# Kernel optimization log

Hardware: AMD Instinct MI355X
Metric: run time of the kernel (lower is better)

The kernel has to match this reference:

```python
import jax, jax.numpy as jnp
import numpy as np

B, L, D = 16, 2048, 192  # batch, frames_per_data, units
H, K = 4, 12             # num_heads, key_dim (hardcoded in build())
EPS = 1e-3               # keras LayerNormalization default epsilon


def layer_norm(x, g, b):
    m = jnp.mean(x, axis=-1, keepdims=True)
    v = jnp.mean(jnp.square(x - m), axis=-1, keepdims=True)
    return (x - m) * jax.lax.rsqrt(v + EPS) * g + b


def conv1d_valid(x, w, b):
    # x: [B,L,C], w: [3,Cin,Cout] -> [B,L-2,Cout]
    return jax.lax.conv_general_dilated(
        x, w, window_strides=(1,), padding='VALID',
        dimension_numbers=('NWC', 'WIO', 'NWC')) + b


def setup_inputs() -> dict:
    key = jax.random.key(0)
    ks = jax.random.split(key, 16)
    s = 0.05
    return {
        'x': jax.random.normal(ks[0], (B, L, D), jnp.float32),
        'ln1_g': jnp.ones((D,), jnp.float32),
        'ln1_b': jnp.zeros((D,), jnp.float32),
        'wq': jax.random.normal(ks[1], (D, H, K), jnp.float32) * s,
        'bq': jnp.zeros((H, K), jnp.float32),
        'wk': jax.random.normal(ks[2], (D, H, K), jnp.float32) * s,
        'bk': jnp.zeros((H, K), jnp.float32),
        'wv': jax.random.normal(ks[3], (D, H, K), jnp.float32) * s,
        'bv': jnp.zeros((H, K), jnp.float32),
        'wo': jax.random.normal(ks[4], (H, K, D), jnp.float32) * s,
        'bo': jnp.zeros((D,), jnp.float32),
        'ln2_g': jnp.ones((D,), jnp.float32),
        'ln2_b': jnp.zeros((D,), jnp.float32),
        'c1_w': jax.random.normal(ks[5], (3, D, D), jnp.float32) * s,
        'c1_b': jnp.zeros((D,), jnp.float32),
        'c2_w': jax.random.normal(ks[6], (3, D, D), jnp.float32) * s,
        'c2_b': jnp.zeros((D,), jnp.float32),
    }


def reference(x, ln1_g, ln1_b, wq, bq, wk, bk, wv, bv, wo, bo,
              ln2_g, ln2_b, c1_w, c1_b, c2_w, c2_b):
    # --- LN1 + causal MHA + residual (dropout = identity at inference) ---
    xn = layer_norm(x, ln1_g, ln1_b)
    q = jnp.einsum('bld,dhk->blhk', xn, wq) + bq
    k = jnp.einsum('bld,dhk->blhk', xn, wk) + bk
    v = jnp.einsum('bld,dhk->blhk', xn, wv) + bv
    scores = jnp.einsum('blhk,bmhk->bhlm', q, k) / jnp.sqrt(jnp.float32(K))
    causal = jnp.tril(jnp.ones((L, L), jnp.float32))  # tril(True) mask
    scores = scores + (1.0 - causal) * (-1e9)          # keras additive mask
    attn = jax.nn.softmax(scores, axis=-1)
    ctx = jnp.einsum('bhlm,bmhk->blhk', attn, v)
    mha = jnp.einsum('blhk,hkd->bld', ctx, wo) + bo
    x = x + mha
    # --- LN2 + positionwise Conv1D feedforward + residual ---
    xn = layer_norm(x, ln2_g, ln2_b)
    h = jax.nn.relu(conv1d_valid(xn, c1_w, c1_b))      # [B,L-2,D]
    h = jnp.pad(h, ((0, 0), (1, 1), (0, 0)))           # ZeroPadding1D(1,1)
    h = conv1d_valid(h, c2_w, c2_b)                    # [B,L-2,D]
    h = jnp.pad(h, ((0, 0), (1, 1), (0, 0)))
    return x + h
```

## Files before the change

kernel.cpp:

```cpp
#include <hip/hip_runtime.h>
#include <hip/hip_bf16.h>

#define L_ 2048
#define D_ 192
#define HK_ 48
#define EPS_ 1e-3f
#define SCALE_ 0.28867513459481287f
#define LOG2E_ 1.4426950408889634f

typedef __hip_bfloat16 bf16;
typedef _Float16 f16;
typedef __fp16 hf16x2 __attribute__((ext_vector_type(2)));
typedef _Float16 f16x4 __attribute__((ext_vector_type(4)));
typedef __bf16 bf16x8 __attribute__((ext_vector_type(8)));
typedef float  f32x4  __attribute__((ext_vector_type(4)));

__device__ __forceinline__ float b2f(bf16 x) { return __bfloat162float(x); }
__device__ __forceinline__ bf16 f2b(float x) { return __float2bfloat16(x); }

__global__ __launch_bounds__(256) void k_prep_all(
    const float* __restrict__ c1w, const float* __restrict__ c2w,
    const float* __restrict__ wq, const float* __restrict__ wk, const float* __restrict__ wv,
    const float* __restrict__ bq, const float* __restrict__ bk, const float* __restrict__ bv,
    const float* __restrict__ wo,
    bf16* __restrict__ wrep1, bf16* __restrict__ wrep2,
    bf16* __restrict__ wrepq, float* __restrict__ bias144, bf16* __restrict__ wrepo)
{
    const int i = blockIdx.x * 256 + threadIdx.x;
    if (i < 110592) {
        const int k = i / 192, n = i - k * 192;
        wrep1[((size_t)(k >> 5) * 192 + n) * 32 + (k & 31)] = f2b(c1w[i]);
    } else if (i < 221184) {
        const int j = i - 110592;
        const int k = j / 192, n = j - k * 192;
        wrep2[((size_t)(k >> 5) * 192 + n) * 32 + (k & 31)] = f2b(c2w[j]);
    } else if (i < 248832) {
        const int j = i - 221184;
        const int kb = j / 4608, rem = j % 4608;
        const int n = rem / 32, kk = rem % 32;
        const int k = kb * 32 + kk;
        float v;
        if (n < 48)       v = wq[k * HK_ + n] * (SCALE_ * LOG2E_);
        else if (n < 96)  v = wk[k * HK_ + (n - 48)];
        else              v = wv[k * HK_ + (n - 96)];
        wrepq[j] = f2b(v);
    } else if (i < 248976) {
        const int j = i - 248832;
        bias144[j] = (j < 48) ? bq[j] * (SCALE_ * LOG2E_)
                   : (j < 96) ? bk[j - 48] : bv[j - 96];
    } else if (i < 261264) {
        const int j = i - 248976;
        const int kb = j / 6144, rem = j % 6144;
        const int n = rem / 32, kk = rem % 32;
        const int k = kb * 32 + kk;
        wrepo[j] = f2b(k < 48 ? wo[k * D_ + n] : 0.f);
    }
}

__global__ __launch_bounds__(256, 4) void k_ln_qkv(
    const float* __restrict__ x, const float* __restrict__ g1, const float* __restrict__ b1,
    const bf16* __restrict__ wrep, const float* __restrict__ bias144,
    f16* __restrict__ qo, f16* __restrict__ ko, f16* __restrict__ vt)
{
    __shared__ bf16 xn[32 * 200];
    const int tid = threadIdx.x;
    const int wave = tid >> 6, lane = tid & 63;
    const int rowbase = blockIdx.x * 32;
    const int b = rowbase >> 11;
    const int lrow0 = rowbase & 2047;

    const float gg0 = g1[lane], gg1 = g1[lane + 64], gg2 = g1[lane + 128];
    const float bb0 = b1[lane], bb1 = b1[lane + 64], bb2 = b1[lane + 128];
    for (int i = 0; i < 8; ++i) {
        const int r = wave * 8 + i;
        const float* xp = x + (size_t)(rowbase + r) * D_;
        const float x0 = xp[lane];
        const float x1 = xp[lane + 64];
        const float x2 = xp[lane + 128];
        float s = x0 + x1 + x2;
        float q = x0 * x0 + x1 * x1 + x2 * x2;
        #pragma unroll
        for (int m = 1; m < 64; m <<= 1) {
            s += __shfl_xor(s, m, 64);
            q += __shfl_xor(q, m, 64);
        }
        const float mean = s * (1.0f / 192.0f);
        const float var  = q * (1.0f / 192.0f) - mean * mean;
        const float rs   = rsqrtf(var + EPS_);
        xn[r * 200 + lane]       = f2b((x0 - mean) * rs * gg0 + bb0);
        xn[r * 200 + lane + 64]  = f2b((x1 - mean) * rs * gg1 + bb1);
        xn[r * 200 + lane + 128] = f2b((x2 - mean) * rs * gg2 + bb2);
    }

    if (tid < 128) {
        const int h  = tid >> 5;
        const int vc = 12 + ((tid >> 3) & 3);
        const int p0 = lrow0 + (tid & 7) * 4;
        f16x4 vv;
        vv[0] = vv[1] = vv[2] = vv[3] = (vc == 12) ? (f16)1.0f : (f16)0.0f;
        *(f16x4*)(vt + ((size_t)(b * 4 + h) * 16 + vc) * 2048 + p0) = vv;
    }
    __syncthreads();

    const int l15 = lane & 15, q4 = lane >> 4;
    const int rt = wave >> 1, g = wave & 1;
    const int ntlim = 5 - g;
    f32x4 acc[5];
    #pragma unroll
    for (int nt = 0; nt < 5; ++nt) acc[nt] = (f32x4){0.f, 0.f, 0.f, 0.f};

    const bf16* xrow = xn + (rt * 16 + l15) * 200 + q4 * 8;
    #pragma unroll
    for (int kb = 0; kb < 6; ++kb) {
        const bf16x8 a = *(const bf16x8*)(xrow + kb * 32);
        const bf16* wp = wrep + ((size_t)kb * 144 + l15) * 32 + q4 * 8
                       + (size_t)(g * 5) * 16 * 32;
        #pragma unroll
        for (int nt = 0; nt < 5; ++nt) {
            if (nt < ntlim) {
                const bf16x8 bfr = *(const bf16x8*)(wp + (size_t)nt * 16 * 32);
                acc[nt] = __builtin_amdgcn_mfma_f32_16x16x32_bf16(a, bfr, acc[nt], 0, 0, 0);
            }
        }
    }

    const int rw = rowbase + rt * 16 + q4 * 4;
    #pragma unroll
    for (int nt = 0; nt < 5; ++nt) {
        if (nt < ntlim) {
            const int ntg = g * 5 + nt;
            const int col = ntg * 16 + l15;
            const float bd = bias144[col];
            if (ntg < 3) {
                #pragma unroll
                for (int reg = 0; reg < 4; ++reg)
                    qo[(size_t)(rw + reg) * HK_ + col] = (f16)(acc[nt][reg] + bd);
            } else if (ntg < 6) {
                #pragma unroll
                for (int reg = 0; reg < 4; ++reg)
                    ko[(size_t)(rw + reg) * HK_ + (col - 48)] = (f16)(acc[nt][reg] + bd);
            } else {
                const int vcol = col - 96;
                const int h = vcol / 12, c12 = vcol % 12;
                f16x4 vv;
                #pragma unroll
                for (int reg = 0; reg < 4; ++reg) vv[reg] = (f16)(acc[nt][reg] + bd);
                *(f16x4*)(vt + ((size_t)(b * 4 + h) * 16 + c12) * 2048 +
                          lrow0 + rt * 16 + q4 * 4) = vv;
            }
        }
    }
}

__global__ __launch_bounds__(256, 8) void k_attn_part(
    const f16* __restrict__ qh, const f16* __restrict__ kh, const f16* __restrict__ vt,
    bf16* __restrict__ part_o, float* __restrict__ part_l)
{
    const int tid = threadIdx.x;
    const int wv = tid >> 6, lane = tid & 63;
    const int quad = lane >> 4, l15 = lane & 15;
    const int bh = blockIdx.x / 36;
    int r = blockIdx.x % 36;
    int qt = 0;
    while (r >= qt + 1) { r -= qt + 1; ++qt; }
    const int ks = r;
    const int b = bh >> 2, h = bh & 3;
    const size_t base  = (size_t)b * L_ * HK_ + h * 12;
    const size_t vbase = ((size_t)bh * 16 + l15) * 2048;
    const int kbase = ks * 256;
    const int qbase = qt * 256 + wv * 64;
    const bool diag = (ks == qt);
    const int ktmax = diag ? 4 * (wv + 1) : 16;

    f16x4 Qf[4];
    #pragma unroll
    for (int s = 0; s < 4; ++s) {
        f16x4 v;
        if (quad < 3)
            v = *(const f16x4*)(qh + base + (size_t)(qbase + s * 16 + l15) * HK_ + quad * 4);
        else { v[0] = (f16)LOG2E_; v[1] = 0; v[2] = 0; v[3] = 0; }
        Qf[s] = v;
    }

    f32x4 O[4];
    #pragma unroll
    for (int s = 0; s < 4; ++s) O[s] = (f32x4){0.f, 0.f, 0.f, 0.f};

    for (int g = 0; g < ktmax; g += 2) {
        f16x4 Kg[2], Vg[2];
        #pragma unroll
        for (int u = 0; u < 2; ++u) {
            const int kt = g + u;
            f16x4 kf;
            if (quad < 3)
                kf = *(const f16x4*)(kh + base + (size_t)(kbase + kt * 16 + l15) * HK_ + quad * 4);
            else { kf[0] = (f16)-6.0f; kf[1] = 0; kf[2] = 0; kf[3] = 0; }
            Kg[u] = kf;
            Vg[u] = *(const f16x4*)(vt + vbase + kbase + kt * 16 + quad * 4);
        }
        #pragma unroll
        for (int u = 0; u < 2; ++u) {
            const int k0 = kbase + (g + u) * 16 + quad * 4;
            #pragma unroll
            for (int s = 0; s < 4; ++s) {
                f32x4 sc = (f32x4){0.f, 0.f, 0.f, 0.f};
                sc = __builtin_amdgcn_mfma_f32_16x16x16f16(Kg[u], Qf[s], sc, 0, 0, 0);
                float p0 = __builtin_amdgcn_exp2f(sc[0]);
                float p1 = __builtin_amdgcn_exp2f(sc[1]);
                float p2 = __builtin_amdgcn_exp2f(sc[2]);
                float p3 = __builtin_amdgcn_exp2f(sc[3]);
                if (diag) {
                    const int qg = qbase + s * 16 + l15;
                    p0 = (k0 + 0 <= qg) ? p0 : 0.f;
                    p1 = (k0 + 1 <= qg) ? p1 : 0.f;
                    p2 = (k0 + 2 <= qg) ? p2 : 0.f;
                    p3 = (k0 + 3 <= qg) ? p3 : 0.f;
                }
                const hf16x2 lo = __builtin_amdgcn_cvt_pkrtz(p0, p1);
                const hf16x2 hi = __builtin_amdgcn_cvt_pkrtz(p2, p3);
                f16x4 p;
                p[0] = (f16)lo[0]; p[1] = (f16)lo[1];
                p[2] = (f16)hi[0]; p[3] = (f16)hi[1];
                O[s] = __builtin_amdgcn_mfma_f32_16x16x16f16(p, Vg[u], O[s], 0, 0, 0);
            }
        }
    }

    const size_t pobase = (size_t)(bh * 8 + ks) * 2048;
    #pragma unroll
    for (int s = 0; s < 4; ++s) {
        const int q16 = qbase + s * 16;
        #pragma unroll
        for (int j = 0; j < 4; ++j) {
            const int qq = q16 + quad * 4 + j;
            if (l15 < 12)       part_o[(pobase + qq) * 12 + l15] = f2b(O[s][j]);
            else if (l15 == 12) part_l[pobase + qq] = O[s][j];
        }
    }
}

__global__ __launch_bounds__(256, 4) void k_proj_ln2(
    const float* __restrict__ x, const bf16* __restrict__ part_o,
    const float* __restrict__ part_l, const bf16* __restrict__ wrepo,
    const float* __restrict__ bo, const float* __restrict__ g2,
    const float* __restrict__ lb2, bf16* __restrict__ x2b,
    bf16* __restrict__ xn2b)
{
    __shared__ bf16 ct[32 * 72];
    __shared__ float psum[4][4][4][2];
    const int tid = threadIdx.x;
    const int wave = tid >> 6, lane = tid & 63;
    const int rowbase = blockIdx.x * 32;
    const int b = rowbase >> 11, lrow = rowbase & 2047;
    const int ns = (lrow >> 8) + 1;

    if (tid < 128) {
        const int rr = tid >> 2, h = tid & 3;
        const int q = lrow + rr;
        const bf16* op = part_o + ((size_t)(b * 4 + h) * 8 * 2048 + q) * 12;
        const float* lp = part_l + (size_t)(b * 4 + h) * 8 * 2048 + q;
        float o[12];
        #pragma unroll
        for (int i = 0; i < 12; ++i) o[i] = 0.f;
        float l = 0.f;
        for (int s = 0; s < ns; ++s) {
            l += lp[(size_t)s * 2048];
            #pragma unroll
            for (int i = 0; i < 12; ++i) o[i] += b2f(op[(size_t)s * 2048 * 12 + i]);
        }
        const float inv = 1.0f / l;
        #pragma unroll
        for (int i = 0; i < 12; ++i) ct[rr * 72 + h * 12 + i] = f2b(o[i] * inv);
        const int c0 = 48 + h * 4;
        #pragma unroll
        for (int i = 0; i < 4; ++i) ct[rr * 72 + c0 + i] = f2b(0.f);
    }
    __syncthreads();

    const int l15 = lane & 15, q4 = lane >> 4;
    const int rt = wave >> 1, g = wave & 1;
    f32x4 acc[6];
    #pragma unroll
    for (int j = 0; j < 6; ++j) acc[j] = (f32x4){0.f, 0.f, 0.f, 0.f};
    const bf16* arow = ct + (rt * 16 + l15) * 72 + q4 * 8;
    #pragma unroll
    for (int kb = 0; kb < 2; ++kb) {
        const bf16x8 a = *(const bf16x8*)(arow + kb * 32);
        const bf16* wp = wrepo + ((size_t)kb * 192 + l15) * 32 + q4 * 8
                       + (size_t)(g * 6) * 16 * 32;
        #pragma unroll
        for (int j = 0; j < 6; ++j) {
            const bf16x8 bb = *(const bf16x8*)(wp + (size_t)j * 16 * 32);
            acc[j] = __builtin_amdgcn_mfma_f32_16x16x32_bf16(a, bb, acc[j], 0, 0, 0);
        }
    }

    const int rw0 = rowbase + rt * 16 + q4 * 4;
    float sum[4] = {0.f, 0.f, 0.f, 0.f}, ssum[4] = {0.f, 0.f, 0.f, 0.f};
    #pragma unroll
    for (int j = 0; j < 6; ++j) {
        const int col = (g * 6 + j) * 16 + l15;
        const float bod = bo[col];
        #pragma unroll
        for (int reg = 0; reg < 4; ++reg) {
            const float v = acc[j][reg] + bod + x[(size_t)(rw0 + reg) * D_ + col];
            acc[j][reg] = v;
            x2b[(size_t)(rw0 + reg) * D_ + col] = f2b(v);
            sum[reg] += v; ssum[reg] += v * v;
        }
    }
    #pragma unroll
    for (int m = 1; m <= 8; m <<= 1) {
        #pragma unroll
        for (int reg = 0; reg < 4; ++reg) {
            sum[reg]  += __shfl_xor(sum[reg], m, 64);
            ssum[reg] += __shfl_xor(ssum[reg], m, 64);
        }
    }
    if (l15 == 0) {
        #pragma unroll
        for (int reg = 0; reg < 4; ++reg) {
            psum[wave][q4][reg][0] = sum[reg];
            psum[wave][q4][reg][1] = ssum[reg];
        }
    }
    __syncthreads();
    float mean[4], rs[4];
    #pragma unroll
    for (int reg = 0; reg < 4; ++reg) {
        const float st = sum[reg]  + psum[wave ^ 1][q4][reg][0];
        const float qt2 = ssum[reg] + psum[wave ^ 1][q4][reg][1];
        mean[reg] = st * (1.0f / 192.0f);
        const float var = qt2 * (1.0f / 192.0f) - mean[reg] * mean[reg];
        rs[reg] = rsqrtf(var + EPS_);
    }
    #pragma unroll
    for (int j = 0; j < 6; ++j) {
        const int col = (g * 6 + j) * 16 + l15;
        const float gg = g2[col], bb2 = lb2[col];
        #pragma unroll
        for (int reg = 0; reg < 4; ++reg)
            xn2b[(size_t)(rw0 + reg) * D_ + col] =
                f2b((acc[j][reg] - mean[reg]) * rs[reg] * gg + bb2);
    }
}

#define INROWB 400
#define NIN    36
#define NH     34
#define HTOFF  (NIN * INROWB)
__global__ __launch_bounds__(256, 4) void k_conv_fused(
    const bf16* __restrict__ act, const bf16* __restrict__ w1,
    const float* __restrict__ b1c, const bf16* __restrict__ w2,
    const float* __restrict__ b2c, const bf16* __restrict__ x2b,
    float* __restrict__ outf)
{
    __shared__ __align__(16) char lds[NIN * INROWB + NH * INROWB];

    const int tid = threadIdx.x;
    const int wave = tid >> 6, lane = tid & 63;
    const int m16 = lane & 15, q = lane >> 4;
    const int rowbase = blockIdx.x * 32;
    const int lrow = rowbase & (L_ - 1);

    {
        const bf16* src0 = act + ((long long)rowbase - 2) * D_;
        bf16x8 v[4];
        int dst[4];
        #pragma unroll
        for (int i = 0; i < 4; ++i) {
            const int g = tid + i * 256;
            if (g < 864) {
                v[i] = *(const bf16x8*)(src0 + g * 8);
                const int row = (g * 2731) >> 16;
                dst[i] = row * INROWB + (g - row * 24) * 16;
            }
        }
        #pragma unroll
        for (int i = 0; i < 4; ++i) {
            const int g = tid + i * 256;
            if (g < 864) *(bf16x8*)(lds + dst[i]) = v[i];
        }
    }

    const int laneA = m16 * INROWB + q * 16;
    const int colw = wave * 48;
    float bd1[3], bd2[3];
    #pragma unroll
    for (int j = 0; j < 3; ++j) {
        bd1[j] = b1c[colw + j * 16 + m16];
        bd2[j] = b2c[colw + j * 16 + m16];
    }
    __syncthreads();

    f32x4 acc1[3][3];
    #pragma unroll
    for (int mt = 0; mt < 3; ++mt)
        #pragma unroll
        for (int j = 0; j < 3; ++j) acc1[mt][j] = (f32x4){0.f, 0.f, 0.f, 0.f};

    #define LOADB(w, kb, j) \
        (*(const bf16x8*)((w) + ((size_t)(kb) * 192 + m16) * 32 + q * 8 \
                          + (size_t)(wave * 3 + (j)) * 16 * 32))
    {
        bf16x8 bB[2][3];
        #pragma unroll
        for (int j = 0; j < 3; ++j) bB[0][j] = LOADB(w1, 0, j);
        #pragma unroll
        for (int kb = 0; kb < 18; ++kb) {
            if (kb + 1 < 18) {
                #pragma unroll
                for (int j = 0; j < 3; ++j) bB[(kb + 1) & 1][j] = LOADB(w1, kb + 1, j);
            }
            const int t = kb / 6, c6 = kb % 6;
            bf16x8 a[3];
            #pragma unroll
            for (int mt = 0; mt < 3; ++mt)
                a[mt] = *(const bf16x8*)(lds + laneA + (mt * 16 + t) * INROWB + c6 * 64);
            #pragma unroll
            for (int j = 0; j < 3; ++j)
                #pragma unroll
                for (int mt = 0; mt < 3; ++mt)
                    acc1[mt][j] = __builtin_amdgcn_mfma_f32_16x16x32_bf16(
                        a[mt], bB[kb & 1][j], acc1[mt][j], 0, 0, 0);
        }
    }

    #pragma unroll
    for (int mt = 0; mt < 3; ++mt)
        #pragma unroll
        for (int j = 0; j < 3; ++j)
            #pragma unroll
            for (int reg = 0; reg < 4; ++reg) {
                const int hr = mt * 16 + q * 4 + reg;
                if (hr < NH) {
                    const int hm = lrow + hr - 1;
                    float v = fmaxf(acc1[mt][j][reg] + bd1[j], 0.f);
                    if (hm == 0 || hm == L_ - 1) v = 0.f;
                    *(bf16*)(lds + HTOFF + hr * INROWB + (colw + j * 16 + m16) * 2) = f2b(v);
                }
            }

    float xr[3][2][4];
    #pragma unroll
    for (int j = 0; j < 3; ++j)
        #pragma unroll
        for (int mt = 0; mt < 2; ++mt)
            #pragma unroll
            for (int reg = 0; reg < 4; ++reg)
                xr[j][mt][reg] = b2f(x2b[(size_t)(rowbase + mt * 16 + q * 4 + reg) * D_
                                         + colw + j * 16 + m16]);
    __syncthreads();

    f32x4 acc2[2][3];
    #pragma unroll
    for (int mt = 0; mt < 2; ++mt)
        #pragma unroll
        for (int j = 0; j < 3; ++j) acc2[mt][j] = (f32x4){0.f, 0.f, 0.f, 0.f};
    {
        bf16x8 bB[2][3];
        #pragma unroll
        for (int j = 0; j < 3; ++j) bB[0][j] = LOADB(w2, 0, j);
        #pragma unroll
        for (int kb = 0; kb < 18; ++kb) {
            if (kb + 1 < 18) {
                #pragma unroll
                for (int j = 0; j < 3; ++j) bB[(kb + 1) & 1][j] = LOADB(w2, kb + 1, j);
            }
            const int t = kb / 6, c6 = kb % 6;
            bf16x8 a[2];
            #pragma unroll
            for (int mt = 0; mt < 2; ++mt)
                a[mt] = *(const bf16x8*)(lds + HTOFF + laneA + (mt * 16 + t) * INROWB + c6 * 64);
            #pragma unroll
            for (int j = 0; j < 3; ++j)
                #pragma unroll
                for (int mt = 0; mt < 2; ++mt)
                    acc2[mt][j] = __builtin_amdgcn_mfma_f32_16x16x32_bf16(
                        a[mt], bB[kb & 1][j], acc2[mt][j], 0, 0, 0);
        }
    }
    #undef LOADB

    #pragma unroll
    for (int j = 0; j < 3; ++j)
        #pragma unroll
        for (int mt = 0; mt < 2; ++mt)
            #pragma unroll
            for (int reg = 0; reg < 4; ++reg) {
                const int r = rowbase + mt * 16 + q * 4 + reg;
                const int m = r & (L_ - 1);
                float v = xr[j][mt][reg];
                if (m != 0 && m != L_ - 1) v += acc2[mt][j][reg] + bd2[j];
                outf[(size_t)r * D_ + colw + j * 16 + m16] = v;
            }
}

extern "C" void kernel_launch(void* const* d_in, const int* in_sizes, int n_in,
                              void* d_out, int out_size, void* d_ws, size_t ws_size,
                              hipStream_t stream)
{
    const float* x    = (const float*)d_in[0];
    const float* ln1g = (const float*)d_in[1];
    const float* ln1b = (const float*)d_in[2];
    const float* wq   = (const float*)d_in[3];
    const float* bq   = (const float*)d_in[4];
    const float* wk   = (const float*)d_in[5];
    const float* bk   = (const float*)d_in[6];
    const float* wv   = (const float*)d_in[7];
    const float* bv   = (const float*)d_in[8];
    const float* wo   = (const float*)d_in[9];
    const float* bo   = (const float*)d_in[10];
    const float* ln2g = (const float*)d_in[11];
    const float* ln2b = (const float*)d_in[12];
    const float* c1w  = (const float*)d_in[13];
    const float* c1b  = (const float*)d_in[14];
    const float* c2w  = (const float*)d_in[15];
    const float* c2b  = (const float*)d_in[16];

    const size_t ROWS = (size_t)16 * L_;
    char* ws = (char*)d_ws;
    size_t off = 4096;
    bf16* xn2b = (bf16*)(ws + off); off += ROWS * D_ * 2;
    off += 4096;
    bf16* hpb  = (bf16*)(ws + off); off += ROWS * D_ * 2;
    off += 4096;
    bf16* x2b  = (bf16*)(ws + off); off += ROWS * D_ * 2;
    f16* qb    = (f16*)(ws + off);   off += ROWS * HK_ * 2;
    f16* kb    = (f16*)(ws + off);   off += ROWS * HK_ * 2;
    f16* vt    = (f16*)(ws + off);   off += (size_t)64 * 16 * 2048 * 2;
    bf16* part_o = (bf16*)(ws + off); off += (size_t)64 * 8 * 2048 * 12 * 2;
    float* part_l = (float*)(ws + off); off += (size_t)64 * 8 * 2048 * 4;
    bf16* wrep1 = (bf16*)(ws + off); off += 576 * 192 * 2;
    bf16* wrep2 = (bf16*)(ws + off); off += 576 * 192 * 2;
    bf16* wrepq = (bf16*)(ws + off); off += 6 * 144 * 32 * 2;
    float* bias144 = (float*)(ws + off); off += 144 * 4;
    bf16* wrepo = (bf16*)(ws + off); off += 2 * 192 * 32 * 2;

    (void)hpb;
    k_prep_all   <<<1021, 256, 0, stream>>>(c1w, c2w, wq, wk, wv, bq, bk, bv, wo,
                                            wrep1, wrep2, wrepq, bias144, wrepo);
    k_ln_qkv     <<<1024, 256, 0, stream>>>(x, ln1g, ln1b, wrepq, bias144, qb, kb, vt);
    k_attn_part  <<<64 * 36, 256, 0, stream>>>(qb, kb, vt, part_o, part_l);
    k_proj_ln2   <<<1024, 256, 0, stream>>>(x, part_o, part_l, wrepo, bo, ln2g, ln2b,
                                            x2b, xn2b);
    k_conv_fused <<<1024, 256, 0, stream>>>(xn2b, wrep1, c1b, wrep2, c2b, x2b,
                                            (float*)d_out);
}
```

Measured before the change: 194.3 us.

## Store Q/K head-major and vectorize split-K partial reduction in projection kernel

```diff
diff --git a/kernel.cpp b/kernel.cpp
--- a/kernel.cpp
+++ b/kernel.cpp
@@ -12,6 +12,7 @@
 typedef _Float16 f16;
 typedef __fp16 hf16x2 __attribute__((ext_vector_type(2)));
 typedef _Float16 f16x4 __attribute__((ext_vector_type(4)));
+typedef __bf16 bf16x4 __attribute__((ext_vector_type(4)));
 typedef __bf16 bf16x8 __attribute__((ext_vector_type(8)));
 typedef float  f32x4  __attribute__((ext_vector_type(4)));
 
@@ -124,7 +125,7 @@
         }
     }
 
-    const int rw = rowbase + rt * 16 + q4 * 4;
+    const int lr0 = lrow0 + rt * 16 + q4 * 4;
     #pragma unroll
     for (int nt = 0; nt < 5; ++nt) {
         if (nt < ntlim) {
@@ -132,13 +133,18 @@
             const int col = ntg * 16 + l15;
             const float bd = bias144[col];
             if (ntg < 3) {
+                const int h2 = col / 12, c12 = col - h2 * 12;
                 #pragma unroll
                 for (int reg = 0; reg < 4; ++reg)
-                    qo[(size_t)(rw + reg) * HK_ + col] = (f16)(acc[nt][reg] + bd);
+                    qo[((size_t)(b * 4 + h2) * 2048 + lr0 + reg) * 12 + c12] =
+                        (f16)(acc[nt][reg] + bd);
             } else if (ntg < 6) {
+                const int ck = col - 48;
+                const int h2 = ck / 12, c12 = ck - h2 * 12;
                 #pragma unroll
                 for (int reg = 0; reg < 4; ++reg)
-                    ko[(size_t)(rw + reg) * HK_ + (col - 48)] = (f16)(acc[nt][reg] + bd);
+                    ko[((size_t)(b * 4 + h2) * 2048 + lr0 + reg) * 12 + c12] =
+                        (f16)(acc[nt][reg] + bd);
             } else {
                 const int vcol = col - 96;
                 const int h = vcol / 12, c12 = vcol % 12;
@@ -164,8 +170,7 @@
     int qt = 0;
     while (r >= qt + 1) { r -= qt + 1; ++qt; }
     const int ks = r;
-    const int b = bh >> 2, h = bh & 3;
-    const size_t base  = (size_t)b * L_ * HK_ + h * 12;
+    const size_t base  = (size_t)bh * 2048 * 12;
     const size_t vbase = ((size_t)bh * 16 + l15) * 2048;
     const int kbase = ks * 256;
     const int qbase = qt * 256 + wv * 64;
@@ -177,7 +182,7 @@
     for (int s = 0; s < 4; ++s) {
         f16x4 v;
         if (quad < 3)
-            v = *(const f16x4*)(qh + base + (size_t)(qbase + s * 16 + l15) * HK_ + quad * 4);
+            v = *(const f16x4*)(qh + base + (size_t)(qbase + s * 16 + l15) * 12 + quad * 4);
         else { v[0] = (f16)LOG2E_; v[1] = 0; v[2] = 0; v[3] = 0; }
         Qf[s] = v;
     }
@@ -193,7 +198,7 @@
             const int kt = g + u;
             f16x4 kf;
             if (quad < 3)
-                kf = *(const f16x4*)(kh + base + (size_t)(kbase + kt * 16 + l15) * HK_ + quad * 4);
+                kf = *(const f16x4*)(kh + base + (size_t)(kbase + kt * 16 + l15) * 12 + quad * 4);
             else { kf[0] = (f16)-6.0f; kf[1] = 0; kf[2] = 0; kf[3] = 0; }
             Kg[u] = kf;
             Vg[u] = *(const f16x4*)(vt + vbase + kbase + kt * 16 + quad * 4);
@@ -247,6 +252,7 @@
     bf16* __restrict__ xn2b)
 {
     __shared__ bf16 ct[32 * 72];
+    __shared__ float linv[128];
     __shared__ float psum[4][4][4][2];
     const int tid = threadIdx.x;
     const int wave = tid >> 6, lane = tid & 63;
@@ -254,26 +260,54 @@
     const int b = rowbase >> 11, lrow = rowbase & 2047;
     const int ns = (lrow >> 8) + 1;
 
-    if (tid < 128) {
-        const int rr = tid >> 2, h = tid & 3;
-        const int q = lrow + rr;
-        const bf16* op = part_o + ((size_t)(b * 4 + h) * 8 * 2048 + q) * 12;
-        const float* lp = part_l + (size_t)(b * 4 + h) * 8 * 2048 + q;
-        float o[12];
-        #pragma unroll
-        for (int i = 0; i < 12; ++i) o[i] = 0.f;
+    {
+        const int sub = tid >> 7, pair = tid & 127;
+        const int rr = pair >> 2, h = pair & 3;
+        const size_t sb = (size_t)(b * 4 + h) * 8 * 2048 + lrow + rr;
+        float o[8] = {0.f, 0.f, 0.f, 0.f, 0.f, 0.f, 0.f, 0.f};
         float l = 0.f;
-        for (int s = 0; s < ns; ++s) {
-            l += lp[(size_t)s * 2048];
-            #pragma unroll
-            for (int i = 0; i < 12; ++i) o[i] += b2f(op[(size_t)s * 2048 * 12 + i]);
-        }
-        const float inv = 1.0f / l;
-        #pragma unroll
-        for (int i = 0; i < 12; ++i) ct[rr * 72 + h * 12 + i] = f2b(o[i] * inv);
-        const int c0 = 48 + h * 4;
-        #pragma unroll
-        for (int i = 0; i < 4; ++i) ct[rr * 72 + c0 + i] = f2b(0.f);
+        if (sub == 0) {
+            #pragma unroll
+            for (int s = 0; s < 8; ++s) {
+                if (s < ns) {
+                    const bf16x8 v = *(const bf16x8*)(part_o + (sb + (size_t)s * 2048) * 12);
+                    #pragma unroll
+                    for (int i = 0; i < 8; ++i) o[i] += (float)v[i];
+                }
+            }
+        } else {
+            #pragma unroll
+            for (int s = 0; s < 8; ++s) {
+                if (s < ns) {
+                    l += part_l[sb + (size_t)s * 2048];
+                    const bf16x4 v = *(const bf16x4*)(part_o + (sb + (size_t)s * 2048) * 12 + 8);
+                    #pragma unroll
+                    for (int i = 0; i < 4; ++i) o[i] += (float)v[i];
+                }
+            }
+            linv[pair] = 1.0f / l;
+        }
+        __syncthreads();
+        const float inv = linv[pair];
+        if (sub == 0) {
+            bf16x4 w0, w1;
+            #pragma unroll
+            for (int i = 0; i < 4; ++i) {
+                w0[i] = (__bf16)(o[i] * inv);
+                w1[i] = (__bf16)(o[4 + i] * inv);
+            }
+            *(bf16x4*)(ct + rr * 72 + h * 12)     = w0;
+            *(bf16x4*)(ct + rr * 72 + h * 12 + 4) = w1;
+        } else {
+            bf16x4 w, z;
+            #pragma unroll
+            for (int i = 0; i < 4; ++i) {
+                w[i] = (__bf16)(o[i] * inv);
+                z[i] = (__bf16)0.0f;
+            }
+            *(bf16x4*)(ct + rr * 72 + h * 12 + 8)  = w;
+            *(bf16x4*)(ct + rr * 72 + 48 + h * 4)  = z;
+        }
     }
     __syncthreads();
 
```

Measured after the change: 195.3 us. Within noise of the previous version (+0.5%).

## Replace split-K causal attention with full-row waves and in-kernel normalization

Applied to the files above, without the earlier changes.

```diff
diff --git a/kernel.cpp b/kernel.cpp
--- a/kernel.cpp
+++ b/kernel.cpp
@@ -12,6 +12,7 @@
 typedef _Float16 f16;
 typedef __fp16 hf16x2 __attribute__((ext_vector_type(2)));
 typedef _Float16 f16x4 __attribute__((ext_vector_type(4)));
+typedef __bf16 bf16x4 __attribute__((ext_vector_type(4)));
 typedef __bf16 bf16x8 __attribute__((ext_vector_type(8)));
 typedef float  f32x4  __attribute__((ext_vector_type(4)));
 
@@ -124,7 +125,7 @@
         }
     }
 
-    const int rw = rowbase + rt * 16 + q4 * 4;
+    const int lr0 = lrow0 + rt * 16 + q4 * 4;
     #pragma unroll
     for (int nt = 0; nt < 5; ++nt) {
         if (nt < ntlim) {
@@ -132,13 +133,18 @@
             const int col = ntg * 16 + l15;
             const float bd = bias144[col];
             if (ntg < 3) {
+                const int h2 = col / 12, c12 = col - h2 * 12;
                 #pragma unroll
                 for (int reg = 0; reg < 4; ++reg)
-                    qo[(size_t)(rw + reg) * HK_ + col] = (f16)(acc[nt][reg] + bd);
+                    qo[((size_t)(b * 4 + h2) * 2048 + lr0 + reg) * 12 + c12] =
+                        (f16)(acc[nt][reg] + bd);
             } else if (ntg < 6) {
+                const int ck = col - 48;
+                const int h2 = ck / 12, c12 = ck - h2 * 12;
                 #pragma unroll
                 for (int reg = 0; reg < 4; ++reg)
-                    ko[(size_t)(rw + reg) * HK_ + (col - 48)] = (f16)(acc[nt][reg] + bd);
+                    ko[((size_t)(b * 4 + h2) * 2048 + lr0 + reg) * 12 + c12] =
+                        (f16)(acc[nt][reg] + bd);
             } else {
                 const int vcol = col - 96;
                 const int h = vcol / 12, c12 = vcol % 12;
@@ -152,65 +158,71 @@
     }
 }
 
-__global__ __launch_bounds__(256, 8) void k_attn_part(
+__global__ __launch_bounds__(256, 8) void k_attn(
     const f16* __restrict__ qh, const f16* __restrict__ kh, const f16* __restrict__ vt,
-    bf16* __restrict__ part_o, float* __restrict__ part_l)
+    bf16* __restrict__ ctx)
 {
     const int tid = threadIdx.x;
     const int wv = tid >> 6, lane = tid & 63;
     const int quad = lane >> 4, l15 = lane & 15;
-    const int bh = blockIdx.x / 36;
-    int r = blockIdx.x % 36;
-    int qt = 0;
-    while (r >= qt + 1) { r -= qt + 1; ++qt; }
-    const int ks = r;
+    const int bh = blockIdx.x & 63;
+    const int qtile = 15 - (blockIdx.x >> 6);
     const int b = bh >> 2, h = bh & 3;
-    const size_t base  = (size_t)b * L_ * HK_ + h * 12;
+    const size_t base  = (size_t)bh * 2048 * 12;
     const size_t vbase = ((size_t)bh * 16 + l15) * 2048;
-    const int kbase = ks * 256;
-    const int qbase = qt * 256 + wv * 64;
-    const bool diag = (ks == qt);
-    const int ktmax = diag ? 4 * (wv + 1) : 16;
-
-    f16x4 Qf[4];
-    #pragma unroll
-    for (int s = 0; s < 4; ++s) {
+    const int qw = qtile * 128 + wv * 32;
+    const int q16 = qw >> 4;
+    const int ntot = q16 + 2;
+
+    f16x4 Qf[2];
+    #pragma unroll
+    for (int s = 0; s < 2; ++s) {
         f16x4 v;
         if (quad < 3)
-            v = *(const f16x4*)(qh + base + (size_t)(qbase + s * 16 + l15) * HK_ + quad * 4);
+            v = *(const f16x4*)(qh + base + (size_t)(qw + s * 16 + l15) * 12 + quad * 4);
         else { v[0] = (f16)LOG2E_; v[1] = 0; v[2] = 0; v[3] = 0; }
         Qf[s] = v;
     }
 
-    f32x4 O[4];
-    #pragma unroll
-    for (int s = 0; s < 4; ++s) O[s] = (f32x4){0.f, 0.f, 0.f, 0.f};
-
-    for (int g = 0; g < ktmax; g += 2) {
-        f16x4 Kg[2], Vg[2];
+    f32x4 O[2];
+    O[0] = (f32x4){0.f, 0.f, 0.f, 0.f};
+    O[1] = (f32x4){0.f, 0.f, 0.f, 0.f};
+
+    f16x4 Kg[2], Vg[2];
+    #pragma unroll
+    for (int u = 0; u < 2; ++u) {
+        if (quad < 3)
+            Kg[u] = *(const f16x4*)(kh + base + (size_t)(u * 16 + l15) * 12 + quad * 4);
+        else { Kg[u][0] = (f16)-6.0f; Kg[u][1] = 0; Kg[u][2] = 0; Kg[u][3] = 0; }
+        Vg[u] = *(const f16x4*)(vt + vbase + u * 16 + quad * 4);
+    }
+
+    for (int t = 0; t < ntot; t += 2) {
+        f16x4 Kn[2], Vn[2];
+        if (t + 2 < ntot) {
+            #pragma unroll
+            for (int u = 0; u < 2; ++u) {
+                const int kt = t + 2 + u;
+                if (quad < 3)
+                    Kn[u] = *(const f16x4*)(kh + base + (size_t)(kt * 16 + l15) * 12 + quad * 4);
+                else { Kn[u][0] = (f16)-6.0f; Kn[u][1] = 0; Kn[u][2] = 0; Kn[u][3] = 0; }
+                Vn[u] = *(const f16x4*)(vt + vbase + kt * 16 + quad * 4);
+            }
+        }
+        const bool masked = (t >= q16);
         #pragma unroll
         for (int u = 0; u < 2; ++u) {
-            const int kt = g + u;
-            f16x4 kf;
-            if (quad < 3)
-                kf = *(const f16x4*)(kh + base + (size_t)(kbase + kt * 16 + l15) * HK_ + quad * 4);
-            else { kf[0] = (f16)-6.0f; kf[1] = 0; kf[2] = 0; kf[3] = 0; }
-            Kg[u] = kf;
-            Vg[u] = *(const f16x4*)(vt + vbase + kbase + kt * 16 + quad * 4);
-        }
-        #pragma unroll
-        for (int u = 0; u < 2; ++u) {
-            const int k0 = kbase + (g + u) * 16 + quad * 4;
-            #pragma unroll
-            for (int s = 0; s < 4; ++s) {
+            const int k0 = (t + u) * 16 + quad * 4;
+            #pragma unroll
+            for (int s = 0; s < 2; ++s) {
                 f32x4 sc = (f32x4){0.f, 0.f, 0.f, 0.f};
                 sc = __builtin_amdgcn_mfma_f32_16x16x16f16(Kg[u], Qf[s], sc, 0, 0, 0);
                 float p0 = __builtin_amdgcn_exp2f(sc[0]);
                 float p1 = __builtin_amdgcn_exp2f(sc[1]);
                 float p2 = __builtin_amdgcn_exp2f(sc[2]);
                 float p3 = __builtin_amdgcn_exp2f(sc[3]);
-                if (diag) {
-                    const int qg = qbase + s * 16 + l15;
+                if (masked) {
+                    const int qg = qw + s * 16 + l15;
                     p0 = (k0 + 0 <= qg) ? p0 : 0.f;
                     p1 = (k0 + 1 <= qg) ? p1 : 0.f;
                     p2 = (k0 + 2 <= qg) ? p2 : 0.f;
@@ -224,24 +236,27 @@
                 O[s] = __builtin_amdgcn_mfma_f32_16x16x16f16(p, Vg[u], O[s], 0, 0, 0);
             }
         }
-    }
-
-    const size_t pobase = (size_t)(bh * 8 + ks) * 2048;
-    #pragma unroll
-    for (int s = 0; s < 4; ++s) {
-        const int q16 = qbase + s * 16;
+        Kg[0] = Kn[0]; Kg[1] = Kn[1];
+        Vg[0] = Vn[0]; Vg[1] = Vn[1];
+    }
+
+    const int src = (quad << 4) + 12;
+    #pragma unroll
+    for (int s = 0; s < 2; ++s) {
         #pragma unroll
         for (int j = 0; j < 4; ++j) {
-            const int qq = q16 + quad * 4 + j;
-            if (l15 < 12)       part_o[(pobase + qq) * 12 + l15] = f2b(O[s][j]);
-            else if (l15 == 12) part_l[pobase + qq] = O[s][j];
+            const float li  = __shfl(O[s][j], src, 64);
+            const float inv = __builtin_amdgcn_rcpf(li);
+            if (l15 < 12)
+                ctx[(size_t)(b * 2048 + qw + s * 16 + quad * 4 + j) * 48 + h * 12 + l15]
+                    = f2b(O[s][j] * inv);
         }
     }
 }
 
 __global__ __launch_bounds__(256, 4) void k_proj_ln2(
-    const float* __restrict__ x, const bf16* __restrict__ part_o,
-    const float* __restrict__ part_l, const bf16* __restrict__ wrepo,
+    const float* __restrict__ x, const bf16* __restrict__ ctx,
+    const bf16* __restrict__ wrepo,
     const float* __restrict__ bo, const float* __restrict__ g2,
     const float* __restrict__ lb2, bf16* __restrict__ x2b,
     bf16* __restrict__ xn2b)
@@ -251,29 +266,20 @@
     const int tid = threadIdx.x;
     const int wave = tid >> 6, lane = tid & 63;
     const int rowbase = blockIdx.x * 32;
-    const int b = rowbase >> 11, lrow = rowbase & 2047;
-    const int ns = (lrow >> 8) + 1;
-
-    if (tid < 128) {
-        const int rr = tid >> 2, h = tid & 3;
-        const int q = lrow + rr;
-        const bf16* op = part_o + ((size_t)(b * 4 + h) * 8 * 2048 + q) * 12;
-        const float* lp = part_l + (size_t)(b * 4 + h) * 8 * 2048 + q;
-        float o[12];
-        #pragma unroll
-        for (int i = 0; i < 12; ++i) o[i] = 0.f;
-        float l = 0.f;
-        for (int s = 0; s < ns; ++s) {
-            l += lp[(size_t)s * 2048];
-            #pragma unroll
-            for (int i = 0; i < 12; ++i) o[i] += b2f(op[(size_t)s * 2048 * 12 + i]);
-        }
-        const float inv = 1.0f / l;
-        #pragma unroll
-        for (int i = 0; i < 12; ++i) ct[rr * 72 + h * 12 + i] = f2b(o[i] * inv);
-        const int c0 = 48 + h * 4;
-        #pragma unroll
-        for (int i = 0; i < 4; ++i) ct[rr * 72 + c0 + i] = f2b(0.f);
+
+    {
+        const int row6 = tid / 6, c6 = tid - row6 * 6;
+        if (tid < 192) {
+            const bf16x8 v = *(const bf16x8*)(ctx + (size_t)(rowbase + row6) * 48 + c6 * 8);
+            *(bf16x8*)(ct + row6 * 72 + c6 * 8) = v;
+        }
+        const int rz = tid / 3, cz = tid - rz * 3;
+        if (tid < 96) {
+            bf16x8 z;
+            #pragma unroll
+            for (int i = 0; i < 8; ++i) z[i] = (__bf16)0.0f;
+            *(bf16x8*)(ct + rz * 72 + 48 + cz * 8) = z;
+        }
     }
     __syncthreads();
 
@@ -328,7 +334,7 @@
     float mean[4], rs[4];
     #pragma unroll
     for (int reg = 0; reg < 4; ++reg) {
-        const float st = sum[reg]  + psum[wave ^ 1][q4][reg][0];
+        const float st  = sum[reg]  + psum[wave ^ 1][q4][reg][0];
         const float qt2 = ssum[reg] + psum[wave ^ 1][q4][reg][1];
         mean[reg] = st * (1.0f / 192.0f);
         const float var = qt2 * (1.0f / 192.0f) - mean[reg] * mean[reg];
@@ -345,7 +351,7 @@
     }
 }
 
-#define INROWB 400
+#define INROWB 416
 #define NIN    36
 #define NH     34
 #define HTOFF  (NIN * INROWB)
@@ -529,8 +535,7 @@
     f16* qb    = (f16*)(ws + off);   off += ROWS * HK_ * 2;
     f16* kb    = (f16*)(ws + off);   off += ROWS * HK_ * 2;
     f16* vt    = (f16*)(ws + off);   off += (size_t)64 * 16 * 2048 * 2;
-    bf16* part_o = (bf16*)(ws + off); off += (size_t)64 * 8 * 2048 * 12 * 2;
-    float* part_l = (float*)(ws + off); off += (size_t)64 * 8 * 2048 * 4;
+    bf16* ctx  = (bf16*)(ws + off);  off += ROWS * 48 * 2;
     bf16* wrep1 = (bf16*)(ws + off); off += 576 * 192 * 2;
     bf16* wrep2 = (bf16*)(ws + off); off += 576 * 192 * 2;
     bf16* wrepq = (bf16*)(ws + off); off += 6 * 144 * 32 * 2;
@@ -541,8 +546,8 @@
     k_prep_all   <<<1021, 256, 0, stream>>>(c1w, c2w, wq, wk, wv, bq, bk, bv, wo,
                                             wrep1, wrep2, wrepq, bias144, wrepo);
     k_ln_qkv     <<<1024, 256, 0, stream>>>(x, ln1g, ln1b, wrepq, bias144, qb, kb, vt);
-    k_attn_part  <<<64 * 36, 256, 0, stream>>>(qb, kb, vt, part_o, part_l);
-    k_proj_ln2   <<<1024, 256, 0, stream>>>(x, part_o, part_l, wrepo, bo, ln2g, ln2b,
+    k_attn       <<<1024, 256, 0, stream>>>(qb, kb, vt, ctx);
+    k_proj_ln2   <<<1024, 256, 0, stream>>>(x, ctx, wrepo, bo, ln2g, ln2b,
                                             x2b, xn2b);
     k_conv_fused <<<1024, 256, 0, stream>>>(xn2b, wrep1, c1b, wrep2, c2b, x2b,
                                             (float*)d_out);
```

Result: slower. 219.8 us (+13.1%).
